# Kernel tuning notes

Measured on AMD Instinct MI355X. Metric: run time of the kernel, lower is better.

## Reference

```python
import jax, jax.numpy as jnp
import numpy as np

EMBED = 1024  # point_net_embedding_dim
H1, H2 = 512, 256  # head_hidden_layer_sizes


def _init(key, shape, fan_in):
    return jax.random.normal(key, shape, dtype=jnp.float32) / jnp.sqrt(jnp.float32(fan_in))


def setup_inputs() -> dict:
    key = jax.random.key(0)
    ks = jax.random.split(key, 13)
    B, N = 256, 1024
    x = jax.random.normal(ks[0], (B, N, 3), dtype=jnp.float32)
    # PointNet shared per-point MLP: 3 -> 64 -> 128 -> EMBED (ReLU), max-pool over points
    W1 = _init(ks[1], (3, 64), 3);        b1 = jnp.zeros((64,), jnp.float32)
    W2 = _init(ks[2], (64, 128), 64);     b2 = jnp.zeros((128,), jnp.float32)
    W3 = _init(ks[3], (128, EMBED), 128); b3 = jnp.zeros((EMBED,), jnp.float32)
    # Head MLP: EMBED -> 512 -> 256 -> 9 (no final activation)
    Wh1 = _init(ks[4], (EMBED, H1), EMBED); bh1 = jnp.zeros((H1,), jnp.float32)
    Wh2 = _init(ks[5], (H1, H2), H1);       bh2 = jnp.zeros((H2,), jnp.float32)
    Wh3 = _init(ks[6], (H2, 9), H2);        bh3 = jnp.zeros((9,), jnp.float32)
    return {"x": x, "W1": W1, "b1": b1, "W2": W2, "b2": b2, "W3": W3, "b3": b3,
            "Wh1": Wh1, "bh1": bh1, "Wh2": Wh2, "bh2": bh2, "Wh3": Wh3, "bh3": bh3}


def svd_projection(M):
    # Project raw 3x3 matrices onto SO(3): R = U diag(1,1,det(U V^T)) V^T
    U, S, Vh = jnp.linalg.svd(M, full_matrices=False)
    det = jnp.linalg.det(jnp.einsum('...ij,...jk->...ik', U, Vh))
    d = jnp.stack([jnp.ones_like(det), jnp.ones_like(det), det], axis=-1)  # [..., 3]
    return jnp.einsum('...ij,...j,...jk->...ik', U, d, Vh)


def reference(x, W1, b1, W2, b2, W3, b3, Wh1, bh1, Wh2, bh2, Wh3, bh3):
    # Shared per-point MLP (ReLU), final_activation=ReLU, then max-pool over points
    h = jax.nn.relu(x @ W1 + b1)          # [B, N, 64]
    h = jax.nn.relu(h @ W2 + b2)          # [B, N, 128]
    h = jax.nn.relu(h @ W3 + b3)          # [B, N, EMBED]
    g = jnp.max(h, axis=-2)               # [B, EMBED] global feature
    # Head MLP -> raw 3x3
    z = jax.nn.relu(g @ Wh1 + bh1)
    z = jax.nn.relu(z @ Wh2 + bh2)
    raw = (z @ Wh3 + bh3).reshape(*x.shape[:-2], 3, 3)
    return svd_projection(raw)
```

## Files before the change

kernel.cpp:

```cpp
#include <hip/hip_runtime.h>
#include <math.h>

typedef _Float16 f16;
typedef _Float16 f16x8 __attribute__((ext_vector_type(8)));
typedef float f32x4 __attribute__((ext_vector_type(4)));

#define H2_STRIDE 140

__global__ __launch_bounds__(256) void prep_weights(
    const float* __restrict__ W1, const float* __restrict__ b1,
    const float* __restrict__ W2, const float* __restrict__ W3,
    f16* __restrict__ W2t, f16* __restrict__ W3t, float* __restrict__ wpk)
{
    int idx = blockIdx.x * 256 + threadIdx.x;
    int stride = gridDim.x * 256;
    for (int i = idx; i < 1024 * 128; i += stride) {
        int c = i >> 7, k = i & 127;
        W3t[i] = (f16)W3[k * 1024 + c];
    }
    for (int i = idx; i < 128 * 64; i += stride) {
        int c = i >> 6, k = i & 63;
        W2t[i] = (f16)W2[k * 128 + c];
    }
    if (idx < 256) {
        int k = idx >> 2, c = idx & 3;
        wpk[idx] = (c < 3) ? W1[c * 64 + k] : b1[k];
    }
}

__global__ __launch_bounds__(512, 2) void pointnet_fused(
    const float* __restrict__ x,
    const float* __restrict__ wpk,
    const f16* __restrict__ W2t,
    const float* __restrict__ b2,
    const f16* __restrict__ W3t,
    const float* __restrict__ b3,
    float* __restrict__ g)
{
    __shared__ float xs[1024 * 3];
    __shared__ __align__(16) float wls[288];
    __shared__ float b2s[128];
    __shared__ __align__(16) f16 h2s[2][128 * H2_STRIDE];

    int b = blockIdx.x;
    int tid = threadIdx.x;
    int lane = tid & 63, w = tid >> 6;
    int lrow = lane & 15, quad = lane >> 4;
    int wr2 = w & 3, wc2 = w >> 2;

    f16x8 bf3[8][4];
    {
        const f16* base = W3t + (size_t)(w * 128 + lrow) * 128 + quad * 8;
#pragma unroll
        for (int ct = 0; ct < 8; ct++)
#pragma unroll
            for (int kc = 0; kc < 4; kc++)
                bf3[ct][kc] = *(const f16x8*)(base + ct * 16 * 128 + kc * 32);
    }
    f16x8 bf2[4][2];
    {
        const f16* base = W2t + (size_t)(wc2 * 64 + lrow) * 64 + quad * 8;
#pragma unroll
        for (int ct = 0; ct < 4; ct++)
#pragma unroll
            for (int kc2 = 0; kc2 < 2; kc2++)
                bf2[ct][kc2] = *(const f16x8*)(base + ct * 16 * 64 + kc2 * 32);
    }

    {
        const float* xb = x + (size_t)b * 3072;
        for (int i = tid; i < 3072; i += 512) xs[i] = xb[i];
        if (tid < 256) {
            int k = tid >> 2, c = tid & 3;
            wls[(k + (k >> 3)) * 4 + c] = wpk[tid];
        }
        if (tid >= 256 && tid < 384) b2s[tid - 256] = b2[tid - 256];
    }
    __syncthreads();

    const f32x4 z4 = {0.f, 0.f, 0.f, 0.f};
    float cmax[8];
#pragma unroll
    for (int ct = 0; ct < 8; ct++) cmax[ct] = -3.0e38f;

    auto phaseA = [&](int chunk) {
        f16* hb = h2s[chunk & 1];
        int p0 = chunk * 128 + wr2 * 32 + lrow;
        float x00 = xs[p0 * 3], x01 = xs[p0 * 3 + 1], x02 = xs[p0 * 3 + 2];
        int p1 = p0 + 16;
        float x10 = xs[p1 * 3], x11 = xs[p1 * 3 + 1], x12 = xs[p1 * 3 + 2];
        f32x4 acc2[2][4];
#pragma unroll
        for (int kc2 = 0; kc2 < 2; kc2++) {
            f16x8 af2[2];
#pragma unroll
            for (int j = 0; j < 8; j++) {
                int k = kc2 * 32 + quad * 8 + j;
                f32x4 wv = *(const f32x4*)&wls[(k + (k >> 3)) * 4];
                float v0 = fmaf(x02, wv[2], fmaf(x01, wv[1], fmaf(x00, wv[0], wv[3])));
                float v1 = fmaf(x12, wv[2], fmaf(x11, wv[1], fmaf(x10, wv[0], wv[3])));
                af2[0][j] = (f16)fmaxf(v0, 0.f);
                af2[1][j] = (f16)fmaxf(v1, 0.f);
            }
#pragma unroll
            for (int rt = 0; rt < 2; rt++)
#pragma unroll
                for (int ct = 0; ct < 4; ct++)
                    acc2[rt][ct] = __builtin_amdgcn_mfma_f32_16x16x32_f16(
                        af2[rt], bf2[ct][kc2], kc2 ? acc2[rt][ct] : z4, 0, 0, 0);
        }
#pragma unroll
        for (int rt = 0; rt < 2; rt++)
#pragma unroll
            for (int ct = 0; ct < 4; ct++) {
                int col = wc2 * 64 + ct * 16 + lrow;
                float bb = b2s[col];
                int rowb = wr2 * 32 + rt * 16 + quad * 4;
#pragma unroll
                for (int r = 0; r < 4; r++)
                    hb[(rowb + r) * H2_STRIDE + col] = (f16)fmaxf(acc2[rt][ct][r] + bb, 0.f);
            }
    };

    auto phaseB = [&](int chunk) {
        const f16* hb = h2s[chunk & 1];
#pragma unroll
        for (int rt = 0; rt < 8; rt++) {
            f32x4 acc[8];
#pragma unroll
            for (int kc = 0; kc < 4; kc++) {
                f16x8 af = *(const f16x8*)(hb + (rt * 16 + lrow) * H2_STRIDE + kc * 32 + quad * 8);
#pragma unroll
                for (int ct = 0; ct < 8; ct++)
                    acc[ct] = __builtin_amdgcn_mfma_f32_16x16x32_f16(
                        af, bf3[ct][kc], kc ? acc[ct] : z4, 0, 0, 0);
            }
#pragma unroll
            for (int ct = 0; ct < 8; ct++) {
                float m01 = fmaxf(acc[ct][0], acc[ct][1]);
                float m23 = fmaxf(acc[ct][2], acc[ct][3]);
                cmax[ct] = fmaxf(cmax[ct], fmaxf(m01, m23));
            }
        }
    };

    phaseA(0);
    __syncthreads();
#pragma unroll 1
    for (int c = 0; c < 7; c++) {
        phaseA(c + 1);
        phaseB(c);
        __syncthreads();
    }
    phaseB(7);

#pragma unroll
    for (int ct = 0; ct < 8; ct++) {
        cmax[ct] = fmaxf(cmax[ct], __shfl_xor(cmax[ct], 16, 64));
        cmax[ct] = fmaxf(cmax[ct], __shfl_xor(cmax[ct], 32, 64));
    }
    if (quad == 0) {
#pragma unroll
        for (int ct = 0; ct < 8; ct++) {
            int cg = w * 128 + ct * 16 + lrow;
            g[(size_t)b * 1024 + cg] = fmaxf(cmax[ct] + b3[cg], 0.f);
        }
    }
}

__device__ inline void jrot(double S[3][3], double V[3][3], int p, int q)
{
    double apq = S[p][q];
    if (fabs(apq) < 1e-36) return;
    double tau = (S[q][q] - S[p][p]) / (2.0 * apq);
    double t = (tau >= 0.0 ? 1.0 : -1.0) / (fabs(tau) + sqrt(1.0 + tau * tau));
    double c = 1.0 / sqrt(1.0 + t * t);
    double s = t * c;
    for (int k = 0; k < 3; k++) {
        double skp = S[k][p], skq = S[k][q];
        S[k][p] = c * skp - s * skq;  S[k][q] = s * skp + c * skq;
    }
    for (int k = 0; k < 3; k++) {
        double spk = S[p][k], sqk = S[q][k];
        S[p][k] = c * spk - s * sqk;  S[q][k] = s * spk + c * sqk;
    }
    for (int k = 0; k < 3; k++) {
        double vkp = V[k][p], vkq = V[k][q];
        V[k][p] = c * vkp - s * vkq;  V[k][q] = s * vkp + c * vkq;
    }
}

__device__ void svd_so3(const float* Mf, float* Rout)
{
    double M[3][3], S[3][3], V[3][3];
    for (int i = 0; i < 3; i++)
        for (int j = 0; j < 3; j++) M[i][j] = (double)Mf[3 * i + j];
    for (int i = 0; i < 3; i++)
        for (int j = 0; j < 3; j++)
            S[i][j] = M[0][i] * M[0][j] + M[1][i] * M[1][j] + M[2][i] * M[2][j];
    for (int i = 0; i < 3; i++)
        for (int j = 0; j < 3; j++) V[i][j] = (i == j) ? 1.0 : 0.0;
    for (int it = 0; it < 10; it++) {
        jrot(S, V, 0, 1); jrot(S, V, 0, 2); jrot(S, V, 1, 2);
    }
    double lam[3] = {S[0][0], S[1][1], S[2][2]};
    int i0 = 0, i1 = 1, i2 = 2, tt;
    if (lam[i0] < lam[i1]) { tt = i0; i0 = i1; i1 = tt; }
    if (lam[i0] < lam[i2]) { tt = i0; i0 = i2; i2 = tt; }
    if (lam[i1] < lam[i2]) { tt = i1; i1 = i2; i2 = tt; }
    double v0[3], v1[3], v2[3];
    for (int k = 0; k < 3; k++) { v0[k] = V[k][i0]; v1[k] = V[k][i1]; v2[k] = V[k][i2]; }
    double u1[3], u2[3], u3[3];
    for (int i = 0; i < 3; i++) u1[i] = M[i][0] * v0[0] + M[i][1] * v0[1] + M[i][2] * v0[2];
    double n1 = sqrt(u1[0] * u1[0] + u1[1] * u1[1] + u1[2] * u1[2]) + 1e-300;
    for (int i = 0; i < 3; i++) u1[i] /= n1;
    for (int i = 0; i < 3; i++) u2[i] = M[i][0] * v1[0] + M[i][1] * v1[1] + M[i][2] * v1[2];
    double d12 = u1[0] * u2[0] + u1[1] * u2[1] + u1[2] * u2[2];
    for (int i = 0; i < 3; i++) u2[i] -= d12 * u1[i];
    double n2 = sqrt(u2[0] * u2[0] + u2[1] * u2[1] + u2[2] * u2[2]) + 1e-300;
    for (int i = 0; i < 3; i++) u2[i] /= n2;
    u3[0] = u1[1] * u2[2] - u1[2] * u2[1];
    u3[1] = u1[2] * u2[0] - u1[0] * u2[2];
    u3[2] = u1[0] * u2[1] - u1[1] * u2[0];
    double c12x = v1[1] * v2[2] - v1[2] * v2[1];
    double c12y = v1[2] * v2[0] - v1[0] * v2[2];
    double c12z = v1[0] * v2[1] - v1[1] * v2[0];
    double detV = v0[0] * c12x + v0[1] * c12y + v0[2] * c12z;
    for (int i = 0; i < 3; i++)
        for (int j = 0; j < 3; j++)
            Rout[3 * i + j] = (float)(u1[i] * v0[j] + u2[i] * v1[j] + detV * u3[i] * v2[j]);
}

__global__ __launch_bounds__(512) void head_one(
    const float* __restrict__ g,
    const float* __restrict__ Wh1, const float* __restrict__ bh1,
    const float* __restrict__ Wh2, const float* __restrict__ bh2,
    const float* __restrict__ Wh3, const float* __restrict__ bh3,
    float* __restrict__ out)
{
    __shared__ float gsm[1024];
    __shared__ float z1p[4][512];
    __shared__ float z1s[512];
    __shared__ float z2p[8][256];
    __shared__ float z2s[256];
    __shared__ float l3p[16][9];
    __shared__ float wh3s[2304];
    __shared__ float raw[12];

    int b = blockIdx.x;
    int tid = threadIdx.x;

    for (int i = tid; i < 1024; i += 512) gsm[i] = g[(size_t)b * 1024 + i];
    for (int i = tid; i < 2304; i += 512) wh3s[i] = Wh3[i];
    __syncthreads();

    {
        int cg = tid & 127;
        int ks = tid >> 7;
        int k0 = ks * 256;
        f32x4 acc = {0.f, 0.f, 0.f, 0.f};
        const float* wp = Wh1 + (size_t)k0 * 512 + cg * 4;
#pragma unroll 8
        for (int k = 0; k < 256; k++) {
            f32x4 wv = *(const f32x4*)(wp + (size_t)k * 512);
            float gk = gsm[k0 + k];
            acc[0] = fmaf(gk, wv[0], acc[0]);
            acc[1] = fmaf(gk, wv[1], acc[1]);
            acc[2] = fmaf(gk, wv[2], acc[2]);
            acc[3] = fmaf(gk, wv[3], acc[3]);
        }
        *(f32x4*)&z1p[ks][cg * 4] = acc;
    }
    __syncthreads();
    {
        float v = bh1[tid & 511];
        int col = tid & 511;
        if (tid < 512) {
            v += z1p[0][col] + z1p[1][col] + z1p[2][col] + z1p[3][col];
            z1s[col] = fmaxf(v, 0.f);
        }
    }
    __syncthreads();

    {
        int cg = tid & 63;
        int ks = tid >> 6;
        int k0 = ks * 64;
        f32x4 acc = {0.f, 0.f, 0.f, 0.f};
        const float* wp = Wh2 + (size_t)k0 * 256 + cg * 4;
#pragma unroll 8
        for (int k = 0; k < 64; k++) {
            f32x4 wv = *(const f32x4*)(wp + (size_t)k * 256);
            float zk = z1s[k0 + k];
            acc[0] = fmaf(zk, wv[0], acc[0]);
            acc[1] = fmaf(zk, wv[1], acc[1]);
            acc[2] = fmaf(zk, wv[2], acc[2]);
            acc[3] = fmaf(zk, wv[3], acc[3]);
        }
        *(f32x4*)&z2p[ks][cg * 4] = acc;
    }
    __syncthreads();
    if (tid < 256) {
        float v = bh2[tid];
#pragma unroll
        for (int j = 0; j < 8; j++) v += z2p[j][tid];
        z2s[tid] = fmaxf(v, 0.f);
    }
    __syncthreads();

    if (tid < 144) {
        int c = tid % 9, ks = tid / 9;
        float a = 0.f;
#pragma unroll
        for (int k = 0; k < 16; k++)
            a = fmaf(z2s[ks * 16 + k], wh3s[(ks * 16 + k) * 9 + c], a);
        l3p[ks][c] = a;
    }
    __syncthreads();
    if (tid < 9) {
        float a = bh3[tid];
#pragma unroll
        for (int j = 0; j < 16; j++) a += l3p[j][tid];
        raw[tid] = a;
    }
    __syncthreads();

    if (tid == 0)
        svd_so3(raw, out + (size_t)b * 9);
}

extern "C" void kernel_launch(void* const* d_in, const int* in_sizes, int n_in,
                              void* d_out, int out_size, void* d_ws, size_t ws_size,
                              hipStream_t stream)
{
    const float* x   = (const float*)d_in[0];
    const float* W1  = (const float*)d_in[1];
    const float* b1  = (const float*)d_in[2];
    const float* W2  = (const float*)d_in[3];
    const float* b2  = (const float*)d_in[4];
    const float* W3  = (const float*)d_in[5];
    const float* b3  = (const float*)d_in[6];
    const float* Wh1 = (const float*)d_in[7];
    const float* bh1 = (const float*)d_in[8];
    const float* Wh2 = (const float*)d_in[9];
    const float* bh2 = (const float*)d_in[10];
    const float* Wh3 = (const float*)d_in[11];
    const float* bh3 = (const float*)d_in[12];
    float* out = (float*)d_out;

    char* ws = (char*)d_ws;
    f16*   W2t = (f16*)ws;
    f16*   W3t = (f16*)(ws + 65536);
    float* wpk = (float*)(ws + 524288);
    float* g   = (float*)(ws + 1048576);

    prep_weights<<<128, 256, 0, stream>>>(W1, b1, W2, W3, W2t, W3t, wpk);
    pointnet_fused<<<256, 512, 0, stream>>>(x, wpk, W2t, b2, W3t, b3, g);
    head_one<<<256, 512, 0, stream>>>(g, Wh1, bh1, Wh2, bh2, Wh3, bh3, out);
}
```

Before: 198.7 us.

## Batch two samples per head block and stagger weight row order

Each block of the head MLP now handles two batch rows, so every Wh1/Wh2 weight vector loaded from global memory is used for two samples. This halves the total weight traffic and the grid size. A per-block rotated starting offset over k spreads concurrent blocks across different weight rows to reduce same-address contention. The pointnet shared-memory stride H2_STRIDE is also changed from 140 to 136, and the SVD projection still runs on only one or two threads per block.

```diff
diff --git a/kernel.cpp b/kernel.cpp
--- a/kernel.cpp
+++ b/kernel.cpp
@@ -5,7 +5,7 @@
 typedef _Float16 f16x8 __attribute__((ext_vector_type(8)));
 typedef float f32x4 __attribute__((ext_vector_type(4)));
 
-#define H2_STRIDE 140
+#define H2_STRIDE 136
 
 __global__ __launch_bounds__(256) void prep_weights(
     const float* __restrict__ W1, const float* __restrict__ b1,
@@ -231,26 +231,28 @@
             Rout[3 * i + j] = (float)(u1[i] * v0[j] + u2[i] * v1[j] + detV * u3[i] * v2[j]);
 }
 
-__global__ __launch_bounds__(512) void head_one(
+__global__ __launch_bounds__(512) void head_batched(
     const float* __restrict__ g,
     const float* __restrict__ Wh1, const float* __restrict__ bh1,
     const float* __restrict__ Wh2, const float* __restrict__ bh2,
     const float* __restrict__ Wh3, const float* __restrict__ bh3,
     float* __restrict__ out)
 {
-    __shared__ float gsm[1024];
-    __shared__ float z1p[4][512];
-    __shared__ float z1s[512];
-    __shared__ float z2p[8][256];
-    __shared__ float z2s[256];
-    __shared__ float l3p[16][9];
+    __shared__ float gsm[2][1024];
+    __shared__ float z1p[4][2][512];
+    __shared__ float z1s[2][512];
+    __shared__ float z2p[8][2][256];
+    __shared__ float z2s[2][256];
+    __shared__ float l3p[16][2][9];
     __shared__ float wh3s[2304];
-    __shared__ float raw[12];
-
-    int b = blockIdx.x;
+    __shared__ float raw[2][12];
+
+    int b0 = blockIdx.x * 2;
     int tid = threadIdx.x;
-
-    for (int i = tid; i < 1024; i += 512) gsm[i] = g[(size_t)b * 1024 + i];
+    int roff = (blockIdx.x * 131) & 255;
+
+    for (int i = tid; i < 2048; i += 512)
+        gsm[i >> 10][i & 1023] = g[(size_t)(b0 + (i >> 10)) * 1024 + (i & 1023)];
     for (int i = tid; i < 2304; i += 512) wh3s[i] = Wh3[i];
     __syncthreads();
 
@@ -258,27 +260,27 @@
         int cg = tid & 127;
         int ks = tid >> 7;
         int k0 = ks * 256;
-        f32x4 acc = {0.f, 0.f, 0.f, 0.f};
-        const float* wp = Wh1 + (size_t)k0 * 512 + cg * 4;
-#pragma unroll 8
-        for (int k = 0; k < 256; k++) {
+        f32x4 a0 = {0.f, 0.f, 0.f, 0.f}, a1 = {0.f, 0.f, 0.f, 0.f};
+        const float* wp = Wh1 + cg * 4;
+#pragma unroll 4
+        for (int kk = 0; kk < 256; kk++) {
+            int k = k0 + ((kk + roff) & 255);
             f32x4 wv = *(const f32x4*)(wp + (size_t)k * 512);
-            float gk = gsm[k0 + k];
-            acc[0] = fmaf(gk, wv[0], acc[0]);
-            acc[1] = fmaf(gk, wv[1], acc[1]);
-            acc[2] = fmaf(gk, wv[2], acc[2]);
-            acc[3] = fmaf(gk, wv[3], acc[3]);
-        }
-        *(f32x4*)&z1p[ks][cg * 4] = acc;
-    }
-    __syncthreads();
-    {
-        float v = bh1[tid & 511];
-        int col = tid & 511;
-        if (tid < 512) {
-            v += z1p[0][col] + z1p[1][col] + z1p[2][col] + z1p[3][col];
-            z1s[col] = fmaxf(v, 0.f);
-        }
+            float g0 = gsm[0][k], g1 = gsm[1][k];
+            a0[0] = fmaf(g0, wv[0], a0[0]);  a1[0] = fmaf(g1, wv[0], a1[0]);
+            a0[1] = fmaf(g0, wv[1], a0[1]);  a1[1] = fmaf(g1, wv[1], a1[1]);
+            a0[2] = fmaf(g0, wv[2], a0[2]);  a1[2] = fmaf(g1, wv[2], a1[2]);
+            a0[3] = fmaf(g0, wv[3], a0[3]);  a1[3] = fmaf(g1, wv[3], a1[3]);
+        }
+        *(f32x4*)&z1p[ks][0][cg * 4] = a0;
+        *(f32x4*)&z1p[ks][1][cg * 4] = a1;
+    }
+    __syncthreads();
+    for (int i = tid; i < 1024; i += 512) {
+        int r = i >> 9, col = i & 511;
+        float v = bh1[col] + z1p[0][r][col] + z1p[1][r][col]
+                           + z1p[2][r][col] + z1p[3][r][col];
+        z1s[r][col] = fmaxf(v, 0.f);
     }
     __syncthreads();
 
@@ -286,47 +288,53 @@
         int cg = tid & 63;
         int ks = tid >> 6;
         int k0 = ks * 64;
-        f32x4 acc = {0.f, 0.f, 0.f, 0.f};
-        const float* wp = Wh2 + (size_t)k0 * 256 + cg * 4;
-#pragma unroll 8
-        for (int k = 0; k < 64; k++) {
+        int roff2 = roff & 63;
+        f32x4 a0 = {0.f, 0.f, 0.f, 0.f}, a1 = {0.f, 0.f, 0.f, 0.f};
+        const float* wp = Wh2 + cg * 4;
+#pragma unroll 4
+        for (int kk = 0; kk < 64; kk++) {
+            int k = k0 + ((kk + roff2) & 63);
             f32x4 wv = *(const f32x4*)(wp + (size_t)k * 256);
-            float zk = z1s[k0 + k];
-            acc[0] = fmaf(zk, wv[0], acc[0]);
-            acc[1] = fmaf(zk, wv[1], acc[1]);
-            acc[2] = fmaf(zk, wv[2], acc[2]);
-            acc[3] = fmaf(zk, wv[3], acc[3]);
-        }
-        *(f32x4*)&z2p[ks][cg * 4] = acc;
-    }
-    __syncthreads();
-    if (tid < 256) {
-        float v = bh2[tid];
-#pragma unroll
-        for (int j = 0; j < 8; j++) v += z2p[j][tid];
-        z2s[tid] = fmaxf(v, 0.f);
-    }
-    __syncthreads();
-
-    if (tid < 144) {
-        int c = tid % 9, ks = tid / 9;
+            float z0 = z1s[0][k], z1v = z1s[1][k];
+            a0[0] = fmaf(z0, wv[0], a0[0]);  a1[0] = fmaf(z1v, wv[0], a1[0]);
+            a0[1] = fmaf(z0, wv[1], a0[1]);  a1[1] = fmaf(z1v, wv[1], a1[1]);
+            a0[2] = fmaf(z0, wv[2], a0[2]);  a1[2] = fmaf(z1v, wv[2], a1[2]);
+            a0[3] = fmaf(z0, wv[3], a0[3]);  a1[3] = fmaf(z1v, wv[3], a1[3]);
+        }
+        *(f32x4*)&z2p[ks][0][cg * 4] = a0;
+        *(f32x4*)&z2p[ks][1][cg * 4] = a1;
+    }
+    __syncthreads();
+    {
+        int r = tid >> 8, col = tid & 255;
+        float v = bh2[col];
+#pragma unroll
+        for (int j = 0; j < 8; j++) v += z2p[j][r][col];
+        z2s[r][col] = fmaxf(v, 0.f);
+    }
+    __syncthreads();
+
+    if (tid < 288) {
+        int r = tid / 144, rem = tid - r * 144;
+        int c = rem % 9, ks = rem / 9;
         float a = 0.f;
 #pragma unroll
         for (int k = 0; k < 16; k++)
-            a = fmaf(z2s[ks * 16 + k], wh3s[(ks * 16 + k) * 9 + c], a);
-        l3p[ks][c] = a;
-    }
-    __syncthreads();
-    if (tid < 9) {
-        float a = bh3[tid];
-#pragma unroll
-        for (int j = 0; j < 16; j++) a += l3p[j][tid];
-        raw[tid] = a;
-    }
-    __syncthreads();
-
-    if (tid == 0)
-        svd_so3(raw, out + (size_t)b * 9);
+            a = fmaf(z2s[r][ks * 16 + k], wh3s[(ks * 16 + k) * 9 + c], a);
+        l3p[ks][r][c] = a;
+    }
+    __syncthreads();
+    if (tid < 18) {
+        int r = tid / 9, c = tid - r * 9;
+        float a = bh3[c];
+#pragma unroll
+        for (int j = 0; j < 16; j++) a += l3p[j][r][c];
+        raw[r][c] = a;
+    }
+    __syncthreads();
+
+    if (tid < 2)
+        svd_so3(&raw[tid][0], out + (size_t)(b0 + tid) * 9);
 }
 
 extern "C" void kernel_launch(void* const* d_in, const int* in_sizes, int n_in,
@@ -356,5 +364,5 @@
 
     prep_weights<<<128, 256, 0, stream>>>(W1, b1, W2, W3, W2t, W3t, wpk);
     pointnet_fused<<<256, 512, 0, stream>>>(x, wpk, W2t, b2, W3t, b3, g);
-    head_one<<<256, 512, 0, stream>>>(g, Wh1, bh1, Wh2, bh2, Wh3, bh3, out);
-}
+    head_batched<<<128, 512, 0, stream>>>(g, Wh1, bh1, Wh2, bh2, Wh3, bh3, out);
+}
```

Result: faster. 172.5 us (-13.2%).
